# Optimization experiments

Measured on AMD Instinct MI355X. Metric: run time of the kernel, lower is better.

The kernel has to match this reference:

```python
import jax, jax.numpy as jnp
import numpy as np

HIDDEN = 128
N_ING = 20000
N_CMP = 10000
N_EDGE = 1000000


def setup_inputs() -> dict:
    key = jax.random.key(0)
    k1, k2, k3, k4, k5, k6, k7 = jax.random.split(key, 7)
    x_ingredient = jax.random.normal(k1, (N_ING, HIDDEN), dtype=jnp.float32)
    x_compound = jax.random.normal(k2, (N_CMP, HIDDEN), dtype=jnp.float32)
    src_idx = jax.random.randint(k3, (N_EDGE,), 0, N_ING)
    dst_idx = jax.random.randint(k4, (N_EDGE,), 0, N_CMP)
    edge_index = jnp.stack([src_idx, dst_idx], axis=0)  # [2, E]
    # Linear(2H, H) then Linear(H, 1), PyTorch default init scale ~ 1/sqrt(fan_in)
    s1 = 1.0 / np.sqrt(2 * HIDDEN)
    s2 = 1.0 / np.sqrt(HIDDEN)
    W1 = jax.random.uniform(k5, (2 * HIDDEN, HIDDEN), dtype=jnp.float32, minval=-s1, maxval=s1)
    b1 = jax.random.uniform(k6, (HIDDEN,), dtype=jnp.float32, minval=-s1, maxval=s1)
    W2 = jax.random.uniform(k7, (HIDDEN, 1), dtype=jnp.float32, minval=-s2, maxval=s2)
    b2 = jnp.zeros((1,), dtype=jnp.float32)
    return {"x_ingredient": x_ingredient, "x_compound": x_compound,
            "edge_index": edge_index, "W1": W1, "b1": b1, "W2": W2, "b2": b2}


def reference(x_ingredient, x_compound, edge_index, W1, b1, W2, b2):
    src = x_ingredient[edge_index[0]]  # [E, H] gather
    dst = x_compound[edge_index[1]]    # [E, H] gather
    h = jnp.concatenate([src, dst], axis=-1)          # [E, 2H]
    h = jax.nn.relu(jnp.dot(h, W1) + b1)              # [E, H]
    out = jax.nn.sigmoid(jnp.dot(h, W2) + b2)         # [E, 1]
    return out
```

## Files before the change

### kernel.cpp

```cpp
#include <hip/hip_runtime.h>


#define H  128
#define NI 20000
#define NC 10000
#define NE 1000000

typedef _Float16 half2v __attribute__((ext_vector_type(2)));
typedef _Float16 half8  __attribute__((ext_vector_type(8)));
typedef float    floatx4 __attribute__((ext_vector_type(4)));

#define P_OFF 0
#define Q_OFF (NI * H)

#define PB (NI / 16)
#define QB (NC / 16)

__launch_bounds__(256)
__global__ void pq_gemm(const float* __restrict__ xin,
                        const float* __restrict__ xcmp,
                        const float* __restrict__ W1,
                        const float* __restrict__ b1,
                        _Float16* __restrict__ ws) {
    const int b    = blockIdx.x;
    const bool isQ = (b >= PB);
    const int  rb  = (isQ ? b - PB : b) * 16;
    const float* X = isQ ? xcmp : xin;
    const int kofs = isQ ? H : 0;
    _Float16* OUT  = ws + (isQ ? Q_OFF : P_OFF);

    const int lane = threadIdx.x & 63;
    const int w    = threadIdx.x >> 6;
    const int quad = lane >> 4;
    const int m    = lane & 15;

    half8 bf[2][4];
    float b1v[2];
#pragma unroll
    for (int nt = 0; nt < 2; ++nt) {
        const int n = w * 32 + nt * 16 + m;
#pragma unroll
        for (int ks = 0; ks < 4; ++ks) {
            const int k0 = kofs + ks * 32 + quad * 8;
#pragma unroll
            for (int j = 0; j < 8; ++j)
                bf[nt][ks][j] = (_Float16)W1[(k0 + j) * H + n];
        }
        b1v[nt] = isQ ? b1[n] : 0.0f;
    }

    half8 af[4];
    const float* xr = X + (long)(rb + m) * H + quad * 8;
#pragma unroll
    for (int ks = 0; ks < 4; ++ks) {
        float4 a = *(const float4*)(xr + ks * 32);
        float4 c = *(const float4*)(xr + ks * 32 + 4);
        half8 v = { (_Float16)a.x, (_Float16)a.y, (_Float16)a.z, (_Float16)a.w,
                    (_Float16)c.x, (_Float16)c.y, (_Float16)c.z, (_Float16)c.w };
        af[ks] = v;
    }

    floatx4 acc[2] = { (floatx4)0.0f, (floatx4)0.0f };
#pragma unroll
    for (int ks = 0; ks < 4; ++ks)
#pragma unroll
        for (int nt = 0; nt < 2; ++nt)
            acc[nt] = __builtin_amdgcn_mfma_f32_16x16x32_f16(af[ks], bf[nt][ks], acc[nt], 0, 0, 0);

#pragma unroll
    for (int nt = 0; nt < 2; ++nt) {
        const int col = w * 32 + nt * 16 + m;
#pragma unroll
        for (int r = 0; r < 4; ++r)
            OUT[(rb + quad * 4 + r) * H + col] = (_Float16)(acc[nt][r] + b1v[nt]);
    }
}

#define EPB   160
#define EGRID (NE / EPB)

__launch_bounds__(256)
__global__ void edge_mlp(const _Float16* __restrict__ ws,
                         const int* __restrict__ src_idx,
                         const int* __restrict__ dst_idx,
                         const float* __restrict__ W2,
                         const float* __restrict__ b2p,
                         float* __restrict__ out) {
    const int tid  = threadIdx.x;
    const int c    = tid & 7;
    const int slot = tid >> 3;

    half2v w2h[8];
    const float* w2c = W2 + c * 16;
#pragma unroll
    for (int j = 0; j < 8; ++j) {
        half2v t = { (_Float16)w2c[2 * j], (_Float16)w2c[2 * j + 1] };
        w2h[j] = t;
    }
    const float b2v = b2p[0];

    int e  = blockIdx.x * EPB + slot;
    int si = src_idx[e];
    int di = dst_idx[e];

#pragma unroll 1
    for (int it = 0; it < 5; ++it) {
        const _Float16* pr = ws + P_OFF + (long)si * H + c * 16;
        const _Float16* qr = ws + Q_OFF + (long)di * H + c * 16;
        half8 p0 = *(const half8*)(pr);
        half8 p1 = *(const half8*)(pr + 8);
        half8 q0 = *(const half8*)(qr);
        half8 q1 = *(const half8*)(qr + 8);

        int si2 = si, di2 = di;
        if (it < 4) { si2 = src_idx[e + 32]; di2 = dst_idx[e + 32]; }

        half8 h0 = p0 + q0;
        half8 h1 = p1 + q1;
        const half8 z = {};
#if __has_builtin(__builtin_elementwise_max)
        h0 = __builtin_elementwise_max(h0, z);
        h1 = __builtin_elementwise_max(h1, z);
#else
#pragma unroll
        for (int j = 0; j < 8; ++j) {
            h0[j] = h0[j] > (_Float16)0 ? h0[j] : (_Float16)0;
            h1[j] = h1[j] > (_Float16)0 ? h1[j] : (_Float16)0;
        }
#endif

        float acc = 0.0f;
#pragma unroll
        for (int j = 0; j < 4; ++j) {
            half2v a = { h0[2 * j], h0[2 * j + 1] };
#if __has_builtin(__builtin_amdgcn_fdot2)
            acc = __builtin_amdgcn_fdot2(a, w2h[j], acc, false);
#else
            acc += (float)a[0] * (float)w2h[j][0] + (float)a[1] * (float)w2h[j][1];
#endif
        }
#pragma unroll
        for (int j = 0; j < 4; ++j) {
            half2v a = { h1[2 * j], h1[2 * j + 1] };
#if __has_builtin(__builtin_amdgcn_fdot2)
            acc = __builtin_amdgcn_fdot2(a, w2h[4 + j], acc, false);
#else
            acc += (float)a[0] * (float)w2h[4 + j][0] + (float)a[1] * (float)w2h[4 + j][1];
#endif
        }

        acc += __shfl_xor(acc, 1);
        acc += __shfl_xor(acc, 2);
        acc += __shfl_xor(acc, 4);

        if (c == 0)
            out[e] = 1.0f / (1.0f + expf(-(acc + b2v)));

        e += 32; si = si2; di = di2;
    }
}

extern "C" void kernel_launch(void* const* d_in, const int* in_sizes, int n_in,
                              void* d_out, int out_size, void* d_ws, size_t ws_size,
                              hipStream_t stream) {
    const float* xin  = (const float*)d_in[0];
    const float* xcmp = (const float*)d_in[1];
    const int*   eidx = (const int*)d_in[2];
    const float* W1   = (const float*)d_in[3];
    const float* b1   = (const float*)d_in[4];
    const float* W2   = (const float*)d_in[5];
    const float* b2   = (const float*)d_in[6];
    float* out = (float*)d_out;
    _Float16* ws = (_Float16*)d_ws;

    hipLaunchKernelGGL(pq_gemm, dim3(PB + QB), dim3(256), 0, stream,
                       xin, xcmp, W1, b1, ws);
    hipLaunchKernelGGL(edge_mlp, dim3(EGRID), dim3(256), 0, stream,
                       ws, eidx, eidx + NE, W2, b2, out);
}
```

Measured before the change: 127.3 us.

## Store P/Q projections in FP8, pre-swizzle W1 fragments, use grid-stride edge loop

The per-node projections P and Q are now stored as FP8 e4m3 instead of FP16, halving the bytes gathered per edge in the edge MLP. The edge kernel decodes them with hardware FP8 converts and accumulates in fp32. A new small kernel pre-converts W1 into MFMA fragment layout so pq_gemm does contiguous half8 loads instead of strided scalar loads. The edge kernel also becomes a persistent grid-stride loop with a fixed grid. The trade-off is lower precision in the hidden activations, which may exceed tolerance, plus one extra kernel launch.

```diff
diff --git a/kernel.cpp b/kernel.cpp
--- a/kernel.cpp
+++ b/kernel.cpp
@@ -6,28 +6,70 @@
 #define NC 10000
 #define NE 1000000
 
-typedef _Float16 half2v __attribute__((ext_vector_type(2)));
-typedef _Float16 half8  __attribute__((ext_vector_type(8)));
+typedef _Float16 half8   __attribute__((ext_vector_type(8)));
+typedef float    floatx2 __attribute__((ext_vector_type(2)));
 typedef float    floatx4 __attribute__((ext_vector_type(4)));
 
-#define P_OFF 0
-#define Q_OFF (NI * H)
+#define P8_OFF    0
+#define Q8_OFF    (NI * H)
+#define WFRAG_B   ((NI + NC) * H)
 
 #define PB (NI / 16)
 #define QB (NC / 16)
+
+#if __has_builtin(__builtin_amdgcn_cvt_pk_f32_fp8) && __has_builtin(__builtin_amdgcn_cvt_pk_fp8_f32)
+#define HW_FP8 1
+#else
+#define HW_FP8 0
+__device__ inline unsigned char enc_e4m3(float x) {
+    unsigned s = x < 0.0f ? 0x80u : 0u;
+    float a = fminf(fabsf(x), 448.0f);
+    if (a < 0.0009765625f) return (unsigned char)s;
+    int e; float m = frexpf(a, &e);
+    int E = e + 6;
+    if (E <= 0) {
+        int f = (int)rintf(a * 512.0f);
+        if (f > 7) return (unsigned char)(s | 0x08);
+        return (unsigned char)(s | f);
+    }
+    int f = (int)rintf((m * 2.0f - 1.0f) * 8.0f);
+    if (f == 8) { f = 0; ++E; }
+    if (E > 15 || (E == 15 && f > 6)) { E = 15; f = 6; }
+    return (unsigned char)(s | (E << 3) | f);
+}
+__device__ inline float dec_e4m3(unsigned char b) {
+    int E = (b >> 3) & 15, f = b & 7;
+    float v = (E == 0) ? (float)f * 0.001953125f
+                       : (float)(8 + f) * exp2f((float)(E - 10));
+    return (b & 0x80) ? -v : v;
+}
+#endif
+
+__launch_bounds__(256)
+__global__ void cvt_w(const float* __restrict__ W1,
+                      unsigned char* __restrict__ wsb) {
+    const int flat = blockIdx.x * 256 + threadIdx.x;
+    const int j    = flat & 7;
+    const int lane = (flat >> 3) & 63;
+    const int ks   = (flat >> 9) & 3;
+    const int ntw  = (flat >> 11) & 7;
+    const int isQ  = (flat >> 14) & 1;
+    const int n = (ntw >> 1) * 32 + (ntw & 1) * 16 + (lane & 15);
+    const int k = isQ * 128 + ks * 32 + (lane >> 4) * 8 + j;
+    ((_Float16*)(wsb + WFRAG_B))[flat] = (_Float16)W1[k * H + n];
+}
 
 __launch_bounds__(256)
 __global__ void pq_gemm(const float* __restrict__ xin,
                         const float* __restrict__ xcmp,
-                        const float* __restrict__ W1,
                         const float* __restrict__ b1,
-                        _Float16* __restrict__ ws) {
+                        unsigned char* __restrict__ wsb) {
     const int b    = blockIdx.x;
     const bool isQ = (b >= PB);
     const int  rb  = (isQ ? b - PB : b) * 16;
     const float* X = isQ ? xcmp : xin;
-    const int kofs = isQ ? H : 0;
-    _Float16* OUT  = ws + (isQ ? Q_OFF : P_OFF);
+    unsigned char* OUT8 = wsb + (isQ ? Q8_OFF : P8_OFF);
+    const _Float16* wfrag = (const _Float16*)(wsb + WFRAG_B);
 
     const int lane = threadIdx.x & 63;
     const int w    = threadIdx.x >> 6;
@@ -38,14 +80,11 @@
     float b1v[2];
 #pragma unroll
     for (int nt = 0; nt < 2; ++nt) {
+        const int ntw = w * 2 + nt;
+#pragma unroll
+        for (int ks = 0; ks < 4; ++ks)
+            bf[nt][ks] = *(const half8*)(wfrag + (((isQ ? 8 : 0) + ntw) * 4 + ks) * 512 + lane * 8);
         const int n = w * 32 + nt * 16 + m;
-#pragma unroll
-        for (int ks = 0; ks < 4; ++ks) {
-            const int k0 = kofs + ks * 32 + quad * 8;
-#pragma unroll
-            for (int j = 0; j < 8; ++j)
-                bf[nt][ks][j] = (_Float16)W1[(k0 + j) * H + n];
-        }
         b1v[nt] = isQ ? b1[n] : 0.0f;
     }
 
@@ -71,16 +110,22 @@
     for (int nt = 0; nt < 2; ++nt) {
         const int col = w * 32 + nt * 16 + m;
 #pragma unroll
-        for (int r = 0; r < 4; ++r)
-            OUT[(rb + quad * 4 + r) * H + col] = (_Float16)(acc[nt][r] + b1v[nt]);
-    }
-}
-
-#define EPB   160
-#define EGRID (NE / EPB)
+        for (int r = 0; r < 4; ++r) {
+            const float v = acc[nt][r] + b1v[nt];
+#if HW_FP8
+            const unsigned u = (unsigned)__builtin_amdgcn_cvt_pk_fp8_f32(v, v, 0, false);
+            OUT8[(rb + quad * 4 + r) * H + col] = (unsigned char)(u & 0xff);
+#else
+            OUT8[(rb + quad * 4 + r) * H + col] = enc_e4m3(v);
+#endif
+        }
+    }
+}
+
+#define EGRID 2048
 
 __launch_bounds__(256)
-__global__ void edge_mlp(const _Float16* __restrict__ ws,
+__global__ void edge_mlp(const unsigned char* __restrict__ wsb,
                          const int* __restrict__ src_idx,
                          const int* __restrict__ dst_idx,
                          const float* __restrict__ W2,
@@ -90,63 +135,47 @@
     const int c    = tid & 7;
     const int slot = tid >> 3;
 
-    half2v w2h[8];
-    const float* w2c = W2 + c * 16;
-#pragma unroll
-    for (int j = 0; j < 8; ++j) {
-        half2v t = { (_Float16)w2c[2 * j], (_Float16)w2c[2 * j + 1] };
-        w2h[j] = t;
-    }
+    float4 w2v[4];
+#pragma unroll
+    for (int i = 0; i < 4; ++i) w2v[i] = *(const float4*)(W2 + c * 16 + i * 4);
     const float b2v = b2p[0];
 
-    int e  = blockIdx.x * EPB + slot;
-    int si = src_idx[e];
-    int di = dst_idx[e];
-
-#pragma unroll 1
-    for (int it = 0; it < 5; ++it) {
-        const _Float16* pr = ws + P_OFF + (long)si * H + c * 16;
-        const _Float16* qr = ws + Q_OFF + (long)di * H + c * 16;
-        half8 p0 = *(const half8*)(pr);
-        half8 p1 = *(const half8*)(pr + 8);
-        half8 q0 = *(const half8*)(qr);
-        half8 q1 = *(const half8*)(qr + 8);
-
-        int si2 = si, di2 = di;
-        if (it < 4) { si2 = src_idx[e + 32]; di2 = dst_idx[e + 32]; }
-
-        half8 h0 = p0 + q0;
-        half8 h1 = p1 + q1;
-        const half8 z = {};
-#if __has_builtin(__builtin_elementwise_max)
-        h0 = __builtin_elementwise_max(h0, z);
-        h1 = __builtin_elementwise_max(h1, z);
+    const unsigned char* P8 = wsb + P8_OFF;
+    const unsigned char* Q8 = wsb + Q8_OFF;
+
+    int e  = blockIdx.x * 32 + slot;
+    int si = 0, di = 0;
+    if (e < NE) { si = src_idx[e]; di = dst_idx[e]; }
+
+    while (e < NE) {
+        const uint4 pd = *(const uint4*)(P8 + si * H + c * 16);
+        const uint4 qd = *(const uint4*)(Q8 + di * H + c * 16);
+
+        const int e2 = e + 32 * EGRID;
+        int si2 = 0, di2 = 0;
+        if (e2 < NE) { si2 = src_idx[e2]; di2 = dst_idx[e2]; }
+
+        float acc = 0.0f;
+        const unsigned pw[4] = { pd.x, pd.y, pd.z, pd.w };
+        const unsigned qw[4] = { qd.x, qd.y, qd.z, qd.w };
+#pragma unroll
+        for (int jw = 0; jw < 4; ++jw) {
+#if HW_FP8
+            floatx2 pl = __builtin_amdgcn_cvt_pk_f32_fp8((int)pw[jw], false);
+            floatx2 ph = __builtin_amdgcn_cvt_pk_f32_fp8((int)pw[jw], true);
+            floatx2 ql = __builtin_amdgcn_cvt_pk_f32_fp8((int)qw[jw], false);
+            floatx2 qh = __builtin_amdgcn_cvt_pk_f32_fp8((int)qw[jw], true);
 #else
-#pragma unroll
-        for (int j = 0; j < 8; ++j) {
-            h0[j] = h0[j] > (_Float16)0 ? h0[j] : (_Float16)0;
-            h1[j] = h1[j] > (_Float16)0 ? h1[j] : (_Float16)0;
-        }
+            floatx2 pl = { dec_e4m3(pw[jw] & 0xff), dec_e4m3((pw[jw] >> 8) & 0xff) };
+            floatx2 ph = { dec_e4m3((pw[jw] >> 16) & 0xff), dec_e4m3(pw[jw] >> 24) };
+            floatx2 ql = { dec_e4m3(qw[jw] & 0xff), dec_e4m3((qw[jw] >> 8) & 0xff) };
+            floatx2 qh = { dec_e4m3((qw[jw] >> 16) & 0xff), dec_e4m3(qw[jw] >> 24) };
 #endif
-
-        float acc = 0.0f;
-#pragma unroll
-        for (int j = 0; j < 4; ++j) {
-            half2v a = { h0[2 * j], h0[2 * j + 1] };
-#if __has_builtin(__builtin_amdgcn_fdot2)
-            acc = __builtin_amdgcn_fdot2(a, w2h[j], acc, false);
-#else
-            acc += (float)a[0] * (float)w2h[j][0] + (float)a[1] * (float)w2h[j][1];
-#endif
-        }
-#pragma unroll
-        for (int j = 0; j < 4; ++j) {
-            half2v a = { h1[2 * j], h1[2 * j + 1] };
-#if __has_builtin(__builtin_amdgcn_fdot2)
-            acc = __builtin_amdgcn_fdot2(a, w2h[4 + j], acc, false);
-#else
-            acc += (float)a[0] * (float)w2h[4 + j][0] + (float)a[1] * (float)w2h[4 + j][1];
-#endif
+            const float4 wv = w2v[jw];
+            acc = fmaf(fmaxf(pl.x + ql.x, 0.0f), wv.x, acc);
+            acc = fmaf(fmaxf(pl.y + ql.y, 0.0f), wv.y, acc);
+            acc = fmaf(fmaxf(ph.x + qh.x, 0.0f), wv.z, acc);
+            acc = fmaf(fmaxf(ph.y + qh.y, 0.0f), wv.w, acc);
         }
 
         acc += __shfl_xor(acc, 1);
@@ -156,7 +185,7 @@
         if (c == 0)
             out[e] = 1.0f / (1.0f + expf(-(acc + b2v)));
 
-        e += 32; si = si2; di = di2;
+        e = e2; si = si2; di = di2;
     }
 }
 
@@ -171,10 +200,10 @@
     const float* W2   = (const float*)d_in[5];
     const float* b2   = (const float*)d_in[6];
     float* out = (float*)d_out;
-    _Float16* ws = (_Float16*)d_ws;
-
-    hipLaunchKernelGGL(pq_gemm, dim3(PB + QB), dim3(256), 0, stream,
-                       xin, xcmp, W1, b1, ws);
-    hipLaunchKernelGGL(edge_mlp, dim3(EGRID), dim3(256), 0, stream,
-                       ws, eidx, eidx + NE, W2, b2, out);
-}
+    unsigned char* wsb = (unsigned char*)d_ws;
+
+    hipLaunchKernelGGL(cvt_w,   dim3(128),     dim3(256), 0, stream, W1, wsb);
+    hipLaunchKernelGGL(pq_gemm, dim3(PB + QB), dim3(256), 0, stream, xin, xcmp, b1, wsb);
+    hipLaunchKernelGGL(edge_mlp, dim3(EGRID),  dim3(256), 0, stream,
+                       wsb, eidx, eidx + NE, W2, b2, out);
+}
```

Result: faster. 114.9 us (-9.7%).
